# Optimization experiments

Measured on AMD Instinct MI355X. Metric: run time of the kernel, lower is better.

## Reference

```python
import jax, jax.numpy as jnp
import numpy as np

N_NODES = 100000
N_EDGES = 1200000
N_GRAPHS = 1024
IN_FEATS = 64
HID = 64
BN_EPS = 1e-5


def setup_inputs() -> dict:
    key = jax.random.key(0)
    ks = jax.random.split(key, 20)
    feats = jax.random.normal(ks[0], (N_NODES, IN_FEATS), jnp.float32)
    src = jax.random.randint(ks[1], (N_EDGES,), 0, N_NODES, jnp.int32)
    dst = jax.random.randint(ks[2], (N_EDGES,), 0, N_NODES, jnp.int32)
    graph_ids = jnp.sort(jax.random.randint(ks[3], (N_NODES,), 0, N_GRAPHS, jnp.int32))

    def lin(k, fi, fo):
        s = 1.0 / np.sqrt(fi)
        kw, kb = jax.random.split(k)
        return (jax.random.uniform(kw, (fi, fo), jnp.float32, -s, s),
                jax.random.uniform(kb, (fo,), jnp.float32, -s, s))

    W_self, _ = lin(ks[4], IN_FEATS, HID)
    W_neigh, b_neigh = lin(ks[5], IN_FEATS, HID)
    W1, b1 = lin(ks[6], HID, 128)
    W2, b2 = lin(ks[7], 128, 64)
    W3, b3 = lin(ks[8], 64, 1)

    def bn(k, d):
        k1, k2, k3, k4 = jax.random.split(k, 4)
        return (jax.random.normal(k1, (d,), jnp.float32) * 0.1 + 1.0,
                jax.random.normal(k2, (d,), jnp.float32) * 0.1,
                jax.random.normal(k3, (d,), jnp.float32) * 0.1,
                jax.random.uniform(k4, (d,), jnp.float32, 0.5, 1.5))

    g1, be1, rm1, rv1 = bn(ks[9], 128)
    g2, be2, rm2, rv2 = bn(ks[10], 64)

    return dict(feats=feats, src=src, dst=dst, graph_ids=graph_ids,
                W_self=W_self, W_neigh=W_neigh, b_neigh=b_neigh,
                W1=W1, b1=b1, g1=g1, be1=be1, rm1=rm1, rv1=rv1,
                W2=W2, b2=b2, g2=g2, be2=be2, rm2=rm2, rv2=rv2,
                W3=W3, b3=b3)


def reference(feats, src, dst, graph_ids, W_self, W_neigh, b_neigh,
              W1, b1, g1, be1, rm1, rv1, W2, b2, g2, be2, rm2, rv2, W3, b3):
    # --- SAGEConv (mean aggregator): h = W_self@h_self + W_neigh@mean_neigh + b
    deg = jax.ops.segment_sum(jnp.ones((src.shape[0],), feats.dtype), dst,
                              num_segments=N_NODES)                      # [N]
    agg = jax.ops.segment_sum(feats[src], dst, num_segments=N_NODES)     # [N, F]
    mean_neigh = agg / jnp.maximum(deg, 1.0)[:, None]
    h = feats @ W_self + mean_neigh @ W_neigh + b_neigh
    h = jax.nn.relu(h)                                                   # activation

    # --- per-graph max readout (dgl.max_nodes)
    hg = jax.ops.segment_max(h, graph_ids, num_segments=N_GRAPHS)        # [G, HID]

    # --- MLP head with eval-mode BatchNorm1d
    def bn(x, g, b, rm, rv):
        return (x - rm) * jax.lax.rsqrt(rv + BN_EPS) * g + b

    x = bn(jax.nn.relu(hg @ W1 + b1), g1, be1, rm1, rv1)
    x = bn(jax.nn.relu(x @ W2 + b2), g2, be2, rm2, rv2)
    return x @ W3 + b3                                                   # [G, n_task]
```

## Files before the change

kernel.cpp:

```cpp
#include <hip/hip_runtime.h>
#include <hip/hip_fp16.h>

#define N_NODES  100000
#define N_EDGES  1200000
#define N_GRAPHS 1024
#define F        64
#define BN_EPS   1e-5f
#define NBUCK    ((N_NODES + 255) / 256)
#define NBLK     512
#define CHUNK    ((N_EDGES + NBLK - 1) / NBLK)
#define MT       128
#define GEMM_BLOCKS ((N_NODES + MT - 1) / MT)
#define CE       3584

__global__ __launch_bounds__(256) void prep(
    const float* __restrict__ feats, const float* __restrict__ Wself,
    const float* __restrict__ Wneigh, __half* __restrict__ Uh,
    __half* __restrict__ Zh, const int* __restrict__ dst,
    int* __restrict__ Ct, int* __restrict__ hgbits) {
  __shared__ __align__(16) char smraw[MT * 65 * 4 + 64 * 128 * 4];
  int t = threadIdx.x;

  if (blockIdx.x >= GEMM_BLOCKS) {
    int* lh = (int*)smraw;
    int b = blockIdx.x - GEMM_BLOCKS;
    int zidx = b * 256 + t;
    if (zidx < N_GRAPHS * F) hgbits[zidx] = 0;
    for (int i = t; i < NBUCK; i += 256) lh[i] = 0;
    __syncthreads();
    int e0 = b * CHUNK, e1 = e0 + CHUNK;
    if (e1 > N_EDGES) e1 = N_EDGES;
    for (int e = e0 + t; e < e1; e += 256) atomicAdd(&lh[dst[e] >> 8], 1);
    __syncthreads();
    for (int i = t; i < NBUCK; i += 256) Ct[(size_t)b * NBUCK + i] = lh[i];
    return;
  }

  float* As = (float*)smraw;
  float* Ws = (float*)(smraw + MT * 65 * 4);
  int mbase = blockIdx.x * MT;

  for (int i = t; i < 64 * 128; i += 256) {
    int k = i >> 7, j = i & 127;
    Ws[i] = (j < 64) ? Wself[k * 64 + j] : Wneigh[k * 64 + (j - 64)];
  }
#pragma unroll
  for (int s = 0; s < 8; s++) {
    int idx = (s * 256 + t) * 4;
    int m = idx >> 6, k = idx & 63;
    int gm = mbase + m;
    float4 v = (gm < N_NODES) ? *(const float4*)(feats + (size_t)gm * F + k)
                              : make_float4(0.f, 0.f, 0.f, 0.f);
    float* d = As + m * 65 + k;
    d[0] = v.x; d[1] = v.y; d[2] = v.z; d[3] = v.w;
  }
  __syncthreads();

  int wave = t >> 6, lane = t & 63;
  int jq = lane & 3, nq = lane >> 2;
  int half = wave & 1;
  int mb = (wave >> 1) * 64 + 4 * nq;
  int joff = half * 64 + jq * 16;

  float acc[4][16];
#pragma unroll
  for (int i = 0; i < 4; i++)
#pragma unroll
    for (int c = 0; c < 16; c++) acc[i][c] = 0.f;

#pragma unroll 4
  for (int k = 0; k < 64; k++) {
    float a0 = As[(mb + 0) * 65 + k];
    float a1 = As[(mb + 1) * 65 + k];
    float a2 = As[(mb + 2) * 65 + k];
    float a3 = As[(mb + 3) * 65 + k];
    const float4* wr = (const float4*)(Ws + k * 128 + joff);
    float4 w4[4];
    w4[0] = wr[0]; w4[1] = wr[1]; w4[2] = wr[2]; w4[3] = wr[3];
    const float* w = (const float*)w4;
#pragma unroll
    for (int c = 0; c < 16; c++) {
      float wv = w[c];
      acc[0][c] += a0 * wv;
      acc[1][c] += a1 * wv;
      acc[2][c] += a2 * wv;
      acc[3][c] += a3 * wv;
    }
  }

  __half* outp = half ? Zh : Uh;
  int jbase = jq * 16;
#pragma unroll
  for (int i = 0; i < 4; i++) {
    int gm = mbase + mb + i;
    if (gm < N_NODES) {
#pragma unroll
      for (int c4 = 0; c4 < 4; c4++) {
        union { __half h[4]; uint2 u; } pk;
        pk.h[0] = __float2half_rn(acc[i][c4 * 4 + 0]);
        pk.h[1] = __float2half_rn(acc[i][c4 * 4 + 1]);
        pk.h[2] = __float2half_rn(acc[i][c4 * 4 + 2]);
        pk.h[3] = __float2half_rn(acc[i][c4 * 4 + 3]);
        *(uint2*)(outp + (size_t)gm * F + jbase + c4 * 4) = pk.u;
      }
    }
  }
}

__global__ __launch_bounds__(NBLK) void cscan(int* __restrict__ Ct,
                                              int* __restrict__ bcnt) {
  __shared__ int s[NBLK];
  int i = blockIdx.x, t = threadIdx.x;
  int v = Ct[(size_t)t * NBUCK + i];
  s[t] = v;
  __syncthreads();
  for (int off = 1; off < NBLK; off <<= 1) {
    int u = (t >= off) ? s[t - off] : 0;
    __syncthreads();
    s[t] += u;
    __syncthreads();
  }
  Ct[(size_t)t * NBUCK + i] = s[t] - v;
  if (t == NBLK - 1) bcnt[i] = s[NBLK - 1];
}

__global__ __launch_bounds__(512) void bscan(const int* __restrict__ bcnt,
                                             int* __restrict__ bstart) {
  __shared__ int s[512];
  int t = threadIdx.x;
  int v = (t < NBUCK) ? bcnt[t] : 0;
  s[t] = v;
  __syncthreads();
  for (int off = 1; off < 512; off <<= 1) {
    int u = (t >= off) ? s[t - off] : 0;
    __syncthreads();
    s[t] += u;
    __syncthreads();
  }
  if (t < NBUCK) bstart[t] = s[t] - v;
  if (t == 0) bstart[NBUCK] = N_EDGES;
}

__global__ __launch_bounds__(256) void cscat(const int* __restrict__ src,
                                             const int* __restrict__ dst,
                                             const int* __restrict__ Ct,
                                             const int* __restrict__ bstart,
                                             int* __restrict__ pairs) {
  __shared__ int cur[NBUCK];
  int b = blockIdx.x, t = threadIdx.x;
  for (int i = t; i < NBUCK; i += 256)
    cur[i] = bstart[i] + Ct[(size_t)b * NBUCK + i];
  __syncthreads();
  int e0 = b * CHUNK, e1 = e0 + CHUNK;
  if (e1 > N_EDGES) e1 = N_EDGES;
  for (int e = e0 + t; e < e1; e += 256) {
    int d = dst[e];
    int pos = atomicAdd(&cur[d >> 8], 1);
    pairs[pos] = (int)((((unsigned)d & 255u) << 24) | (unsigned)src[e]);
  }
}

__global__ __launch_bounds__(1024) void gather_place(
    const __half* __restrict__ Uh, const __half* __restrict__ Zh,
    const int* __restrict__ pairs, const int* __restrict__ bstart,
    const float* __restrict__ bneigh, const int* __restrict__ gids,
    int* __restrict__ hgbits) {
  __shared__ int eidx_l[CE];
  __shared__ int rsl[256];
  __shared__ int lh[256];
  __shared__ int cur[256];
  int b = blockIdx.x, t = threadIdx.x;
  int nb0 = b << 8;
  int r0 = bstart[b], r1 = bstart[b + 1];
  int E = r1 - r0; if (E > CE) E = CE;

  if (t < 256) lh[t] = 0;
  __syncthreads();
  for (int e = t; e < E; e += 1024)
    atomicAdd(&lh[((unsigned)pairs[r0 + e]) >> 24], 1);
  __syncthreads();
  if (t < 256) cur[t] = lh[t];
  __syncthreads();
  for (int off = 1; off < 256; off <<= 1) {
    int u = (t < 256 && t >= off) ? cur[t - off] : 0;
    __syncthreads();
    if (t < 256) cur[t] += u;
    __syncthreads();
  }
  if (t < 256) { int ex = cur[t] - lh[t]; rsl[t] = ex; cur[t] = ex; }
  __syncthreads();
  for (int e = t; e < E; e += 1024) {
    unsigned p = (unsigned)pairs[r0 + e];
    int pos = atomicAdd(&cur[p >> 24], 1);
    eidx_l[pos] = (int)(p & 0xFFFFFFu);
  }
  __syncthreads();

  int wave = t >> 6, lane = t & 63;
  int fl = lane & 15, sub = lane >> 4;
  float4 b4 = *(const float4*)(bneigh + 4 * fl);
  int nl = wave * 16;
  int nend = nl + 16;
  if (nb0 + nl >= N_NODES) return;
  if (nb0 + nend > N_NODES) nend = N_NODES - nb0;

  int curg = gids[nb0 + nl];
  float4 gmax = {0.f, 0.f, 0.f, 0.f};

  for (; nl < nend; nl++) {
    int node = nb0 + nl;
    int rr  = rsl[nl];
    int deg = lh[nl];
    uint2 ur = *(const uint2*)(Uh + (size_t)node * F + 4 * fl);
    float sx = 0.f, sy = 0.f, sz = 0.f, sw = 0.f;
    for (int jj = 0; jj < deg; jj += 16) {
      int j0 = jj + sub;
      int s0 = (j0      < deg) ? eidx_l[rr + j0]      : 0;
      int s1 = (j0 + 4  < deg) ? eidx_l[rr + j0 + 4]  : 0;
      int s2 = (j0 + 8  < deg) ? eidx_l[rr + j0 + 8]  : 0;
      int s3 = (j0 + 12 < deg) ? eidx_l[rr + j0 + 12] : 0;
      uint2 z0 = *(const uint2*)(Zh + (size_t)s0 * F + 4 * fl);
      uint2 z1 = *(const uint2*)(Zh + (size_t)s1 * F + 4 * fl);
      uint2 z2 = *(const uint2*)(Zh + (size_t)s2 * F + 4 * fl);
      uint2 z3 = *(const uint2*)(Zh + (size_t)s3 * F + 4 * fl);
      if (j0 < deg) {
        float2 f0 = __half22float2(*(__half2*)&z0.x);
        float2 f1 = __half22float2(*(__half2*)&z0.y);
        sx += f0.x; sy += f0.y; sz += f1.x; sw += f1.y;
      }
      if (j0 + 4 < deg) {
        float2 f0 = __half22float2(*(__half2*)&z1.x);
        float2 f1 = __half22float2(*(__half2*)&z1.y);
        sx += f0.x; sy += f0.y; sz += f1.x; sw += f1.y;
      }
      if (j0 + 8 < deg) {
        float2 f0 = __half22float2(*(__half2*)&z2.x);
        float2 f1 = __half22float2(*(__half2*)&z2.y);
        sx += f0.x; sy += f0.y; sz += f1.x; sw += f1.y;
      }
      if (j0 + 12 < deg) {
        float2 f0 = __half22float2(*(__half2*)&z3.x);
        float2 f1 = __half22float2(*(__half2*)&z3.y);
        sx += f0.x; sy += f0.y; sz += f1.x; sw += f1.y;
      }
    }
    sx += __shfl_xor(sx, 16); sy += __shfl_xor(sy, 16);
    sz += __shfl_xor(sz, 16); sw += __shfl_xor(sw, 16);
    sx += __shfl_xor(sx, 32); sy += __shfl_xor(sy, 32);
    sz += __shfl_xor(sz, 32); sw += __shfl_xor(sw, 32);
    float inv = 1.0f / fmaxf((float)deg, 1.0f);

    int g = gids[node];
    if (g != curg) {
      if (sub == 0) {
        int* hp = hgbits + (size_t)curg * F + 4 * fl;
        atomicMax(hp + 0, __float_as_int(gmax.x));
        atomicMax(hp + 1, __float_as_int(gmax.y));
        atomicMax(hp + 2, __float_as_int(gmax.z));
        atomicMax(hp + 3, __float_as_int(gmax.w));
      }
      curg = g; gmax = make_float4(0.f, 0.f, 0.f, 0.f);
    }

    float2 uf0 = __half22float2(*(__half2*)&ur.x);
    float2 uf1 = __half22float2(*(__half2*)&ur.y);
    gmax.x = fmaxf(gmax.x, fmaxf(uf0.x + sx * inv + b4.x, 0.f));
    gmax.y = fmaxf(gmax.y, fmaxf(uf0.y + sy * inv + b4.y, 0.f));
    gmax.z = fmaxf(gmax.z, fmaxf(uf1.x + sz * inv + b4.z, 0.f));
    gmax.w = fmaxf(gmax.w, fmaxf(uf1.y + sw * inv + b4.w, 0.f));
  }
  if (sub == 0) {
    int* hp = hgbits + (size_t)curg * F + 4 * fl;
    atomicMax(hp + 0, __float_as_int(gmax.x));
    atomicMax(hp + 1, __float_as_int(gmax.y));
    atomicMax(hp + 2, __float_as_int(gmax.z));
    atomicMax(hp + 3, __float_as_int(gmax.w));
  }
}

#define GPB 8
__global__ __launch_bounds__(128) void mlp(
    const float* __restrict__ hg,
    const float* __restrict__ W1, const float* __restrict__ b1,
    const float* __restrict__ g1, const float* __restrict__ be1,
    const float* __restrict__ rm1, const float* __restrict__ rv1,
    const float* __restrict__ W2, const float* __restrict__ b2,
    const float* __restrict__ g2, const float* __restrict__ be2,
    const float* __restrict__ rm2, const float* __restrict__ rv2,
    const float* __restrict__ W3, const float* __restrict__ b3,
    float* __restrict__ out) {
  __shared__ float W1s[64 * 128];
  __shared__ float W2s[128 * 64];
  __shared__ float W3s[64];
  __shared__ float sc1[128], sh1[128], b1s[128];
  __shared__ float sc2[64],  sh2[64],  b2s[64];
  __shared__ float s0[64], s1[128], s2[64];
  int t = threadIdx.x;

  for (int i = t; i < 64 * 128; i += 128) W1s[i] = W1[i];
  for (int i = t; i < 128 * 64; i += 128) W2s[i] = W2[i];
  if (t < 64) W3s[t] = W3[t];
  {
    float iv = rsqrtf(rv1[t] + BN_EPS);
    float sc = g1[t] * iv;
    sc1[t] = sc; sh1[t] = be1[t] - rm1[t] * sc; b1s[t] = b1[t];
  }
  if (t < 64) {
    float iv = rsqrtf(rv2[t] + BN_EPS);
    float sc = g2[t] * iv;
    sc2[t] = sc; sh2[t] = be2[t] - rm2[t] * sc; b2s[t] = b2[t];
  }
  __syncthreads();

  for (int gg = 0; gg < GPB; gg++) {
    int g = blockIdx.x * GPB + gg;
    if (t < 64) s0[t] = hg[(size_t)g * F + t];
    __syncthreads();
    {
      float acc = b1s[t];
      for (int i = 0; i < 64; i++) acc += s0[i] * W1s[i * 128 + t];
      acc = fmaxf(acc, 0.0f);
      s1[t] = acc * sc1[t] + sh1[t];
    }
    __syncthreads();
    if (t < 64) {
      float acc = b2s[t];
      for (int i = 0; i < 128; i++) acc += s1[i] * W2s[i * 64 + t];
      acc = fmaxf(acc, 0.0f);
      s2[t] = acc * sc2[t] + sh2[t];
    }
    __syncthreads();
    if (t < 64) {
      float p = s2[t] * W3s[t];
      for (int off = 32; off > 0; off >>= 1) p += __shfl_down(p, off);
      if (t == 0) out[g] = p + b3[0];
    }
    __syncthreads();
  }
}

extern "C" void kernel_launch(void* const* d_in, const int* in_sizes, int n_in,
                              void* d_out, int out_size, void* d_ws, size_t ws_size,
                              hipStream_t stream) {
  const float* feats  = (const float*)d_in[0];
  const int*   src    = (const int*)d_in[1];
  const int*   dst    = (const int*)d_in[2];
  const int*   gids   = (const int*)d_in[3];
  const float* Wself  = (const float*)d_in[4];
  const float* Wneigh = (const float*)d_in[5];
  const float* bneigh = (const float*)d_in[6];
  const float* W1  = (const float*)d_in[7];
  const float* b1  = (const float*)d_in[8];
  const float* g1  = (const float*)d_in[9];
  const float* be1 = (const float*)d_in[10];
  const float* rm1 = (const float*)d_in[11];
  const float* rv1 = (const float*)d_in[12];
  const float* W2  = (const float*)d_in[13];
  const float* b2  = (const float*)d_in[14];
  const float* g2  = (const float*)d_in[15];
  const float* be2 = (const float*)d_in[16];
  const float* rm2 = (const float*)d_in[17];
  const float* rv2 = (const float*)d_in[18];
  const float* W3  = (const float*)d_in[19];
  const float* b3  = (const float*)d_in[20];

  __half* Uh   = (__half*)d_ws;
  __half* Zh   = Uh + (size_t)N_NODES * F;
  int* bstart  = (int*)(Zh + (size_t)N_NODES * F);
  int* bcnt    = bstart + (NBUCK + 1);
  int* hgbits  = bcnt + NBUCK;
  int* Ct      = hgbits + (size_t)N_GRAPHS * F;
  int* pairs   = Ct + (size_t)NBLK * NBUCK;

  prep<<<GEMM_BLOCKS + NBLK, 256, 0, stream>>>(feats, Wself, Wneigh, Uh, Zh,
                                               dst, Ct, hgbits);
  cscan<<<NBUCK, NBLK, 0, stream>>>(Ct, bcnt);
  bscan<<<1, 512, 0, stream>>>(bcnt, bstart);
  cscat<<<NBLK, 256, 0, stream>>>(src, dst, Ct, bstart, pairs);
  gather_place<<<NBUCK, 1024, 0, stream>>>(Uh, Zh, pairs, bstart, bneigh,
                                           gids, hgbits);
  mlp<<<N_GRAPHS / GPB, 128, 0, stream>>>((const float*)hgbits,
                                          W1, b1, g1, be1, rm1, rv1,
                                          W2, b2, g2, be2, rm2, rv2, W3, b3,
                                          (float*)d_out);
}
```

Measured before the change: 226.9 us.

## Use fp16 MFMA for node feature projection GEMM in prep kernel

Replaces the scalar fp32 FMA GEMM (feats times [W_self|W_neigh]) with MFMA 16x16x32 f16 instructions. Features and weights are converted to fp16 into padded LDS tiles, which also roughly halves shared memory use. Precision of the inputs drops to fp16, though outputs were already stored as fp16. The GEMM is only one stage among several kernels (histogram, scan, scatter, readout), so its share of total time bounds the benefit.

```diff
diff --git a/kernel.cpp b/kernel.cpp
--- a/kernel.cpp
+++ b/kernel.cpp
@@ -12,13 +12,17 @@
 #define MT       128
 #define GEMM_BLOCKS ((N_NODES + MT - 1) / MT)
 #define CE       3584
+#define LDA      72
+
+typedef _Float16 f16x8 __attribute__((ext_vector_type(8)));
+typedef float f32x4 __attribute__((ext_vector_type(4)));
 
 __global__ __launch_bounds__(256) void prep(
     const float* __restrict__ feats, const float* __restrict__ Wself,
     const float* __restrict__ Wneigh, __half* __restrict__ Uh,
     __half* __restrict__ Zh, const int* __restrict__ dst,
     int* __restrict__ Ct, int* __restrict__ hgbits) {
-  __shared__ __align__(16) char smraw[MT * 65 * 4 + 64 * 128 * 4];
+  __shared__ __align__(16) char smraw[2 * 128 * LDA * 2];
   int t = threadIdx.x;
 
   if (blockIdx.x >= GEMM_BLOCKS) {
@@ -36,72 +40,81 @@
     return;
   }
 
-  float* As = (float*)smraw;
-  float* Ws = (float*)(smraw + MT * 65 * 4);
+  __half* As = (__half*)smraw;
+  __half* Bs = As + 128 * LDA;
   int mbase = blockIdx.x * MT;
 
-  for (int i = t; i < 64 * 128; i += 256) {
-    int k = i >> 7, j = i & 127;
-    Ws[i] = (j < 64) ? Wself[k * 64 + j] : Wneigh[k * 64 + (j - 64)];
-  }
 #pragma unroll
   for (int s = 0; s < 8; s++) {
-    int idx = (s * 256 + t) * 4;
-    int m = idx >> 6, k = idx & 63;
-    int gm = mbase + m;
-    float4 v = (gm < N_NODES) ? *(const float4*)(feats + (size_t)gm * F + k)
+    int idx = s * 256 + t;
+    int row = idx >> 4, c4 = idx & 15;
+    int gm = mbase + row;
+    float4 v = (gm < N_NODES) ? *(const float4*)(feats + (size_t)gm * F + c4 * 4)
                               : make_float4(0.f, 0.f, 0.f, 0.f);
-    float* d = As + m * 65 + k;
-    d[0] = v.x; d[1] = v.y; d[2] = v.z; d[3] = v.w;
+    union { __half h[4]; uint2 u; } pk;
+    pk.h[0] = __float2half_rn(v.x); pk.h[1] = __float2half_rn(v.y);
+    pk.h[2] = __float2half_rn(v.z); pk.h[3] = __float2half_rn(v.w);
+    *(uint2*)(As + row * LDA + c4 * 4) = pk.u;
+  }
+
+#pragma unroll
+  for (int s = 0; s < 2; s++) {
+    int unit = s * 256 + t;
+    int kq = unit >> 5, c4 = unit & 31;
+    const float* Wp = (c4 < 16) ? (Wself + c4 * 4) : (Wneigh + (c4 - 16) * 4);
+    float4 w0 = *(const float4*)(Wp + (kq * 4 + 0) * 64);
+    float4 w1 = *(const float4*)(Wp + (kq * 4 + 1) * 64);
+    float4 w2 = *(const float4*)(Wp + (kq * 4 + 2) * 64);
+    float4 w3 = *(const float4*)(Wp + (kq * 4 + 3) * 64);
+    float a[4][4] = {{w0.x, w0.y, w0.z, w0.w}, {w1.x, w1.y, w1.z, w1.w},
+                     {w2.x, w2.y, w2.z, w2.w}, {w3.x, w3.y, w3.z, w3.w}};
+#pragma unroll
+    for (int c = 0; c < 4; c++) {
+      union { __half h[4]; uint2 u; } pk;
+      pk.h[0] = __float2half_rn(a[0][c]); pk.h[1] = __float2half_rn(a[1][c]);
+      pk.h[2] = __float2half_rn(a[2][c]); pk.h[3] = __float2half_rn(a[3][c]);
+      *(uint2*)(Bs + (c4 * 4 + c) * LDA + kq * 4) = pk.u;
+    }
   }
   __syncthreads();
 
   int wave = t >> 6, lane = t & 63;
-  int jq = lane & 3, nq = lane >> 2;
-  int half = wave & 1;
-  int mb = (wave >> 1) * 64 + 4 * nq;
-  int joff = half * 64 + jq * 16;
-
-  float acc[4][16];
-#pragma unroll
-  for (int i = 0; i < 4; i++)
-#pragma unroll
-    for (int c = 0; c < 16; c++) acc[i][c] = 0.f;
-
-#pragma unroll 4
-  for (int k = 0; k < 64; k++) {
-    float a0 = As[(mb + 0) * 65 + k];
-    float a1 = As[(mb + 1) * 65 + k];
-    float a2 = As[(mb + 2) * 65 + k];
-    float a3 = As[(mb + 3) * 65 + k];
-    const float4* wr = (const float4*)(Ws + k * 128 + joff);
-    float4 w4[4];
-    w4[0] = wr[0]; w4[1] = wr[1]; w4[2] = wr[2]; w4[3] = wr[3];
-    const float* w = (const float*)w4;
-#pragma unroll
-    for (int c = 0; c < 16; c++) {
-      float wv = w[c];
-      acc[0][c] += a0 * wv;
-      acc[1][c] += a1 * wv;
-      acc[2][c] += a2 * wv;
-      acc[3][c] += a3 * wv;
-    }
-  }
-
-  __half* outp = half ? Zh : Uh;
-  int jbase = jq * 16;
-#pragma unroll
-  for (int i = 0; i < 4; i++) {
-    int gm = mbase + mb + i;
-    if (gm < N_NODES) {
-#pragma unroll
-      for (int c4 = 0; c4 < 4; c4++) {
+  int lr = lane & 15, kg = lane >> 4;
+  int r0 = wave * 32;
+
+  f32x4 acc[2][8];
+#pragma unroll
+  for (int i = 0; i < 2; i++)
+#pragma unroll
+    for (int j = 0; j < 8; j++) acc[i][j] = (f32x4){0.f, 0.f, 0.f, 0.f};
+
+#pragma unroll
+  for (int h = 0; h < 2; h++) {
+    f16x8 a0 = *(const f16x8*)(As + (r0 + lr) * LDA + h * 32 + kg * 8);
+    f16x8 a1 = *(const f16x8*)(As + (r0 + 16 + lr) * LDA + h * 32 + kg * 8);
+#pragma unroll
+    for (int j = 0; j < 8; j++) {
+      f16x8 wv = *(const f16x8*)(Bs + (j * 16 + lr) * LDA + h * 32 + kg * 8);
+      acc[0][j] = __builtin_amdgcn_mfma_f32_16x16x32_f16(wv, a0, acc[0][j], 0, 0, 0);
+      acc[1][j] = __builtin_amdgcn_mfma_f32_16x16x32_f16(wv, a1, acc[1][j], 0, 0, 0);
+    }
+  }
+
+#pragma unroll
+  for (int i = 0; i < 2; i++) {
+    int node = mbase + r0 + i * 16 + lr;
+    if (node < N_NODES) {
+#pragma unroll
+      for (int j = 0; j < 8; j++) {
+        int f = j * 16 + kg * 4;
         union { __half h[4]; uint2 u; } pk;
-        pk.h[0] = __float2half_rn(acc[i][c4 * 4 + 0]);
-        pk.h[1] = __float2half_rn(acc[i][c4 * 4 + 1]);
-        pk.h[2] = __float2half_rn(acc[i][c4 * 4 + 2]);
-        pk.h[3] = __float2half_rn(acc[i][c4 * 4 + 3]);
-        *(uint2*)(outp + (size_t)gm * F + jbase + c4 * 4) = pk.u;
+        pk.h[0] = __float2half_rn(acc[i][j][0]);
+        pk.h[1] = __float2half_rn(acc[i][j][1]);
+        pk.h[2] = __float2half_rn(acc[i][j][2]);
+        pk.h[3] = __float2half_rn(acc[i][j][3]);
+        __half* outp = (f < 64) ? (Uh + (size_t)node * F + f)
+                                : (Zh + (size_t)node * F + (f - 64));
+        *(uint2*)outp = pk.u;
       }
     }
   }
```

New measurement: 212.8 us. 6.2% less time.
